# Kernel optimization log

Measured on AMD Instinct MI355X. Metric: run time of the kernel, lower is better.

The kernel has to match this reference:

```python
import jax, jax.numpy as jnp
import numpy as np

SCALE = 16.0 / 8.0  # alpha / rank


def setup_inputs() -> dict:
    key = jax.random.key(0)
    ks = jax.random.split(key, 5)
    d_in, d_out, rank = 4096, 4096, 8
    x = jax.random.normal(ks[0], (4, 2048, d_in), dtype=jnp.float32)
    base_weight = jax.random.normal(ks[1], (d_out, d_in), dtype=jnp.float32) * 0.02
    lora_A = jax.random.normal(ks[2], (rank, d_in), dtype=jnp.float32) * 0.02
    lora_B = jax.random.normal(ks[3], (d_out, rank), dtype=jnp.float32) * 0.02
    bias = jax.random.normal(ks[4], (d_out,), dtype=jnp.float32) * 0.02
    return {"x": x, "base_weight": base_weight, "lora_A": lora_A,
            "lora_B": lora_B, "bias": bias}


def reference(x, base_weight, lora_A, lora_B, bias):
    # weight = base + scale * (B @ A)   -> [d_out, d_in]
    weight = base_weight + SCALE * (lora_B @ lora_A)
    # F.linear: x @ weight.T + bias
    return jnp.einsum('bsi,oi->bso', x, weight) + bias
```

## Files before the change

kernel.cpp:

```cpp
#include <hip/hip_runtime.h>
#include <hip/hip_bf16.h>
#include <cstdio>


using bf16   = __bf16;
using bf16x8 = __attribute__((ext_vector_type(8))) __bf16;
using f32x4  = __attribute__((ext_vector_type(4))) float;

#define BM 256
#define BN 256
#define BK 64
#define WXBLK 2048

__global__ __launch_bounds__(256) void prep_fused(
    const float* __restrict__ x, const float* __restrict__ base,
    const float* __restrict__ A, const float* __restrict__ Bm,
    bf16* __restrict__ Xb, bf16* __restrict__ Wb,
    long n8x, int K, int rank, float scale) {
    if (blockIdx.x < WXBLK) {
        const long stride = (long)WXBLK * 256;
        for (long i = (long)blockIdx.x * 256 + threadIdx.x; i < n8x; i += stride) {
            const float4 a = reinterpret_cast<const float4*>(x)[2 * i];
            const float4 b = reinterpret_cast<const float4*>(x)[2 * i + 1];
            bf16x8 o;
            o[0] = (bf16)a.x; o[1] = (bf16)a.y; o[2] = (bf16)a.z; o[3] = (bf16)a.w;
            o[4] = (bf16)b.x; o[5] = (bf16)b.y; o[6] = (bf16)b.z; o[7] = (bf16)b.w;
            reinterpret_cast<bf16x8*>(Xb)[i] = o;
        }
    } else {
        const int o = blockIdx.x - WXBLK;
        float br[8];
        const int rr = rank < 8 ? rank : 8;
        for (int r = 0; r < rr; ++r) br[r] = scale * Bm[(size_t)o * rank + r];

        const float* brow = base + (size_t)o * K;
        bf16*        wrow = Wb + (size_t)o * K;

        for (int c = threadIdx.x * 8; c < K; c += 256 * 8) {
            float4 s0 = *reinterpret_cast<const float4*>(brow + c);
            float4 s1 = *reinterpret_cast<const float4*>(brow + c + 4);
            if (rank == 8) {
#pragma unroll
                for (int r = 0; r < 8; ++r) {
                    const float4 a0 = *reinterpret_cast<const float4*>(A + (size_t)r * K + c);
                    const float4 a1 = *reinterpret_cast<const float4*>(A + (size_t)r * K + c + 4);
                    s0.x += br[r] * a0.x; s0.y += br[r] * a0.y;
                    s0.z += br[r] * a0.z; s0.w += br[r] * a0.w;
                    s1.x += br[r] * a1.x; s1.y += br[r] * a1.y;
                    s1.z += br[r] * a1.z; s1.w += br[r] * a1.w;
                }
            } else {
                for (int r = 0; r < rank; ++r) {
                    const float b = scale * Bm[(size_t)o * rank + r];
                    const float4 a0 = *reinterpret_cast<const float4*>(A + (size_t)r * K + c);
                    const float4 a1 = *reinterpret_cast<const float4*>(A + (size_t)r * K + c + 4);
                    s0.x += b * a0.x; s0.y += b * a0.y; s0.z += b * a0.z; s0.w += b * a0.w;
                    s1.x += b * a1.x; s1.y += b * a1.y; s1.z += b * a1.z; s1.w += b * a1.w;
                }
            }
            bf16x8 ov;
            ov[0] = (bf16)s0.x; ov[1] = (bf16)s0.y; ov[2] = (bf16)s0.z; ov[3] = (bf16)s0.w;
            ov[4] = (bf16)s1.x; ov[5] = (bf16)s1.y; ov[6] = (bf16)s1.z; ov[7] = (bf16)s1.w;
            *reinterpret_cast<bf16x8*>(wrow + c) = ov;
        }
    }
}

__global__ __launch_bounds__(512, 2) void gemm_2reg(
    const bf16* __restrict__ Xb,
    const bf16* __restrict__ Wb,
    const float* __restrict__ bias,
    float* __restrict__ out,
    int M, int N, int K)
{
    __shared__ __align__(16) bf16 As[2 * 2 * 256 * 32];
    __shared__ __align__(16) bf16 Bs[2 * 2 * 256 * 32];

    const int tid  = threadIdx.x;
    const int lane = tid & 63;
    const int wv   = tid >> 6;
    const int wm   = wv >> 2;
    const int wn   = wv & 3;

    const int nbx = gridDim.x;
    const int nwg = gridDim.x * gridDim.y;
    const int orig = blockIdx.y * nbx + blockIdx.x;
    const int swz = ((nwg & 7) == 0) ? ((orig & 7) * (nwg >> 3) + (orig >> 3)) : orig;
    const int m0 = (swz / nbx) * BM;
    const int n0 = (swz % nbx) * BN;

    const int r16 = lane & 15;
    const int q   = lane >> 4;
    const int cq  = (q ^ ((r16 >> 1) & 3)) * 8;

    const bf16* srcA[2];
    const bf16* srcB[2];
#pragma unroll
    for (int i = 0; i < 2; ++i) {
        const int slot = i * 512 + tid;
        const int row  = slot >> 2;
        const int c    = (tid & 3) ^ ((row >> 1) & 3);
        srcA[i] = Xb + (size_t)(m0 + row) * K + c * 8;
        srcB[i] = Wb + (size_t)(n0 + row) * K + c * 8;
    }
    const int dst0 = (0 * 512 + wv * 64) * 8;
    const int dst1 = (1 * 512 + wv * 64) * 8;

#define STAGE_A(buf, kh, koff)                                                        \
    do {                                                                              \
        __builtin_amdgcn_global_load_lds(                                             \
            (const __attribute__((address_space(1))) void*)(srcA[0] + (koff) + (kh) * 32), \
            (__attribute__((address_space(3))) void*)(As + (buf) * 16384 + (kh) * 8192 + dst0), \
            16, 0, 0);                                                                \
        __builtin_amdgcn_global_load_lds(                                             \
            (const __attribute__((address_space(1))) void*)(srcA[1] + (koff) + (kh) * 32), \
            (__attribute__((address_space(3))) void*)(As + (buf) * 16384 + (kh) * 8192 + dst1), \
            16, 0, 0);                                                                \
    } while (0)
#define STAGE_B(buf, kh, koff)                                                        \
    do {                                                                              \
        __builtin_amdgcn_global_load_lds(                                             \
            (const __attribute__((address_space(1))) void*)(srcB[0] + (koff) + (kh) * 32), \
            (__attribute__((address_space(3))) void*)(Bs + (buf) * 16384 + (kh) * 8192 + dst0), \
            16, 0, 0);                                                                \
        __builtin_amdgcn_global_load_lds(                                             \
            (const __attribute__((address_space(1))) void*)(srcB[1] + (koff) + (kh) * 32), \
            (__attribute__((address_space(3))) void*)(Bs + (buf) * 16384 + (kh) * 8192 + dst1), \
            16, 0, 0);                                                                \
    } while (0)

    int aoff[2][4], boff[4];
#pragma unroll
    for (int mh = 0; mh < 2; ++mh)
#pragma unroll
        for (int f = 0; f < 4; ++f)
            aoff[mh][f] = (wm * 128 + mh * 64 + f * 16 + r16) * 32 + cq;
#pragma unroll
    for (int f = 0; f < 4; ++f)
        boff[f] = (wn * 64 + f * 16 + r16) * 32 + cq;

    f32x4 acc[8][4] = {};

    const int NT = K / BK;

    STAGE_A(0, 0, 0);
    STAGE_B(0, 0, 0);
    STAGE_A(0, 1, 0);
    STAGE_B(0, 1, 0);
    if (NT > 1) {
        STAGE_A(1, 0, BK);
        STAGE_B(1, 0, BK);
        asm volatile("s_waitcnt vmcnt(8)" ::: "memory");
    } else {
        asm volatile("s_waitcnt vmcnt(4)" ::: "memory");
    }
    __builtin_amdgcn_s_barrier();

    for (int t = 0; t < NT; ++t) {
        const int cur   = t & 1;
        const int nxt   = cur ^ 1;
        const int koff1 = (t + 1) * BK;
        const int koff2 = (t + 2) * BK;
        const bool pre1 = (t + 1 < NT);
        const bool pre2 = (t + 2 < NT);
        bf16x8 bf[4], af0[4], af1[4];

        {
            const bf16* Ab = As + cur * 16384;
            const bf16* Bb = Bs + cur * 16384;
#pragma unroll
            for (int f = 0; f < 4; ++f) bf[f]  = *reinterpret_cast<const bf16x8*>(Bb + boff[f]);
#pragma unroll
            for (int f = 0; f < 4; ++f) af0[f] = *reinterpret_cast<const bf16x8*>(Ab + aoff[0][f]);
#pragma unroll
            for (int f = 0; f < 4; ++f) af1[f] = *reinterpret_cast<const bf16x8*>(Ab + aoff[1][f]);
            if (pre1) { STAGE_A(nxt, 1, koff1); STAGE_B(nxt, 1, koff1); }
            asm volatile("s_waitcnt lgkmcnt(4)" ::: "memory");
            __builtin_amdgcn_sched_barrier(0);
            __builtin_amdgcn_s_setprio(1);
#pragma unroll
            for (int f = 0; f < 4; ++f)
#pragma unroll
                for (int n = 0; n < 4; ++n)
                    acc[f][n] = __builtin_amdgcn_mfma_f32_16x16x32_bf16(af0[f], bf[n], acc[f][n], 0, 0, 0);
            __builtin_amdgcn_s_setprio(0);
            asm volatile("s_waitcnt lgkmcnt(0)" ::: "memory");
            __builtin_amdgcn_sched_barrier(0);
            __builtin_amdgcn_s_setprio(1);
#pragma unroll
            for (int f = 0; f < 4; ++f)
#pragma unroll
                for (int n = 0; n < 4; ++n)
                    acc[4 + f][n] = __builtin_amdgcn_mfma_f32_16x16x32_bf16(af1[f], bf[n], acc[4 + f][n], 0, 0, 0);
            __builtin_amdgcn_s_setprio(0);
            if (t == NT - 1) asm volatile("s_waitcnt vmcnt(0)" ::: "memory");
            else             asm volatile("s_waitcnt vmcnt(8)" ::: "memory");
            __builtin_amdgcn_s_barrier();
        }
        {
            const bf16* Ab = As + cur * 16384 + 8192;
            const bf16* Bb = Bs + cur * 16384 + 8192;
#pragma unroll
            for (int f = 0; f < 4; ++f) bf[f]  = *reinterpret_cast<const bf16x8*>(Bb + boff[f]);
#pragma unroll
            for (int f = 0; f < 4; ++f) af0[f] = *reinterpret_cast<const bf16x8*>(Ab + aoff[0][f]);
#pragma unroll
            for (int f = 0; f < 4; ++f) af1[f] = *reinterpret_cast<const bf16x8*>(Ab + aoff[1][f]);
            if (pre2) { STAGE_A(cur, 0, koff2); STAGE_B(cur, 0, koff2); }
            asm volatile("s_waitcnt lgkmcnt(4)" ::: "memory");
            __builtin_amdgcn_sched_barrier(0);
            __builtin_amdgcn_s_setprio(1);
#pragma unroll
            for (int f = 0; f < 4; ++f)
#pragma unroll
                for (int n = 0; n < 4; ++n)
                    acc[f][n] = __builtin_amdgcn_mfma_f32_16x16x32_bf16(af0[f], bf[n], acc[f][n], 0, 0, 0);
            __builtin_amdgcn_s_setprio(0);
            asm volatile("s_waitcnt lgkmcnt(0)" ::: "memory");
            __builtin_amdgcn_sched_barrier(0);
            __builtin_amdgcn_s_setprio(1);
#pragma unroll
            for (int f = 0; f < 4; ++f)
#pragma unroll
                for (int n = 0; n < 4; ++n)
                    acc[4 + f][n] = __builtin_amdgcn_mfma_f32_16x16x32_bf16(af1[f], bf[n], acc[4 + f][n], 0, 0, 0);
            __builtin_amdgcn_s_setprio(0);
            if (t == NT - 2)     asm volatile("s_waitcnt vmcnt(4)" ::: "memory");
            else if (t < NT - 2) asm volatile("s_waitcnt vmcnt(8)" ::: "memory");
            if (t < NT - 1) __builtin_amdgcn_s_barrier();
        }
    }

#pragma unroll
    for (int mf = 0; mf < 8; ++mf) {
        const int gr = m0 + wm * 128 + (mf >> 2) * 64 + (mf & 3) * 16 + q * 4;
#pragma unroll
        for (int nf = 0; nf < 4; ++nf) {
            const int gc = n0 + wn * 64 + nf * 16 + r16;
            const float bv = bias[gc];
#pragma unroll
            for (int r = 0; r < 4; ++r)
                out[(size_t)(gr + r) * N + gc] = acc[mf][nf][r] + bv;
        }
    }
#undef STAGE_A
#undef STAGE_B
}

extern "C" void kernel_launch(void* const* d_in, const int* in_sizes, int n_in,
                              void* d_out, int out_size, void* d_ws, size_t ws_size,
                              hipStream_t stream) {
    const float* x    = (const float*)d_in[0];
    const float* base = (const float*)d_in[1];
    const float* lA   = (const float*)d_in[2];
    const float* lB   = (const float*)d_in[3];
    const float* bias = (const float*)d_in[4];
    float* out = (float*)d_out;

    const int  N    = in_sizes[4];
    const int  rank = in_sizes[3] / N;
    const int  K    = in_sizes[2] / rank;
    const long M    = (long)in_sizes[0] / K;
    const float scale = 16.0f / (float)rank;

    bf16* Xb = (bf16*)d_ws;
    bf16* Wb = Xb + (size_t)M * K;
    const size_t need = ((size_t)M * K + (size_t)N * K) * sizeof(bf16);
    if (ws_size < need) {
        fprintf(stderr, "kernel_launch: ws_size %zu < needed %zu\n", ws_size, need);
        return;
    }

    const long n8x = (long)M * K / 8;
    prep_fused<<<dim3((unsigned)(WXBLK + N)), dim3(256), 0, stream>>>(
        x, base, lA, lB, Xb, Wb, n8x, K, rank, scale);

    gemm_2reg<<<dim3(N / BN, (unsigned)(M / BM)), dim3(512), 0, stream>>>(
        Xb, Wb, bias, out, (int)M, N, K);
}
```

Before: 553.3 us.

## Double-buffer LDS fragment registers to overlap next half-tile reads with MFMA

Restructures the GEMM main loop so each half-K step reads the next half-tile's A/B fragments from LDS into a second register set while the current set feeds the MFMAs. The lgkmcnt/vmcnt waits and barrier placement change to match the new order. The aim is to hide LDS read latency behind matrix math instead of stalling between the two MFMA groups. It doubles fragment register usage (24 bf16x8 registers), which risks register pressure at the 512x2 launch bounds. It also depends on correct manual waitcnt accounting.

```diff
diff --git a/kernel.cpp b/kernel.cpp
--- a/kernel.cpp
+++ b/kernel.cpp
@@ -66,7 +66,7 @@
     }
 }
 
-__global__ __launch_bounds__(512, 2) void gemm_2reg(
+__global__ __launch_bounds__(512, 2) void gemm_rp(
     const bf16* __restrict__ Xb,
     const bf16* __restrict__ Wb,
     const float* __restrict__ bias,
@@ -140,6 +140,8 @@
         boff[f] = (wn * 64 + f * 16 + r16) * 32 + cq;
 
     f32x4 acc[8][4] = {};
+    bf16x8 b0[4], a00[4], a01[4];
+    bf16x8 b1[4], a10[4], a11[4];
 
     const int NT = K / BK;
 
@@ -150,11 +152,21 @@
     if (NT > 1) {
         STAGE_A(1, 0, BK);
         STAGE_B(1, 0, BK);
-        asm volatile("s_waitcnt vmcnt(8)" ::: "memory");
+        asm volatile("s_waitcnt vmcnt(4)" ::: "memory");
     } else {
-        asm volatile("s_waitcnt vmcnt(4)" ::: "memory");
+        asm volatile("s_waitcnt vmcnt(0)" ::: "memory");
     }
     __builtin_amdgcn_s_barrier();
+    {
+        const bf16* Ab = As;
+        const bf16* Bb = Bs;
+#pragma unroll
+        for (int f = 0; f < 4; ++f) b0[f]  = *reinterpret_cast<const bf16x8*>(Bb + boff[f]);
+#pragma unroll
+        for (int f = 0; f < 4; ++f) a00[f] = *reinterpret_cast<const bf16x8*>(Ab + aoff[0][f]);
+#pragma unroll
+        for (int f = 0; f < 4; ++f) a01[f] = *reinterpret_cast<const bf16x8*>(Ab + aoff[1][f]);
+    }
 
     for (int t = 0; t < NT; ++t) {
         const int cur   = t & 1;
@@ -163,71 +175,72 @@
         const int koff2 = (t + 2) * BK;
         const bool pre1 = (t + 1 < NT);
         const bool pre2 = (t + 2 < NT);
-        bf16x8 bf[4], af0[4], af1[4];
-
-        {
-            const bf16* Ab = As + cur * 16384;
-            const bf16* Bb = Bs + cur * 16384;
-#pragma unroll
-            for (int f = 0; f < 4; ++f) bf[f]  = *reinterpret_cast<const bf16x8*>(Bb + boff[f]);
-#pragma unroll
-            for (int f = 0; f < 4; ++f) af0[f] = *reinterpret_cast<const bf16x8*>(Ab + aoff[0][f]);
-#pragma unroll
-            for (int f = 0; f < 4; ++f) af1[f] = *reinterpret_cast<const bf16x8*>(Ab + aoff[1][f]);
-            if (pre1) { STAGE_A(nxt, 1, koff1); STAGE_B(nxt, 1, koff1); }
-            asm volatile("s_waitcnt lgkmcnt(4)" ::: "memory");
-            __builtin_amdgcn_sched_barrier(0);
-            __builtin_amdgcn_s_setprio(1);
-#pragma unroll
-            for (int f = 0; f < 4; ++f)
-#pragma unroll
-                for (int n = 0; n < 4; ++n)
-                    acc[f][n] = __builtin_amdgcn_mfma_f32_16x16x32_bf16(af0[f], bf[n], acc[f][n], 0, 0, 0);
-            __builtin_amdgcn_s_setprio(0);
-            asm volatile("s_waitcnt lgkmcnt(0)" ::: "memory");
-            __builtin_amdgcn_sched_barrier(0);
-            __builtin_amdgcn_s_setprio(1);
-#pragma unroll
-            for (int f = 0; f < 4; ++f)
-#pragma unroll
-                for (int n = 0; n < 4; ++n)
-                    acc[4 + f][n] = __builtin_amdgcn_mfma_f32_16x16x32_bf16(af1[f], bf[n], acc[4 + f][n], 0, 0, 0);
-            __builtin_amdgcn_s_setprio(0);
-            if (t == NT - 1) asm volatile("s_waitcnt vmcnt(0)" ::: "memory");
-            else             asm volatile("s_waitcnt vmcnt(8)" ::: "memory");
-            __builtin_amdgcn_s_barrier();
-        }
+
         {
             const bf16* Ab = As + cur * 16384 + 8192;
             const bf16* Bb = Bs + cur * 16384 + 8192;
 #pragma unroll
-            for (int f = 0; f < 4; ++f) bf[f]  = *reinterpret_cast<const bf16x8*>(Bb + boff[f]);
-#pragma unroll
-            for (int f = 0; f < 4; ++f) af0[f] = *reinterpret_cast<const bf16x8*>(Ab + aoff[0][f]);
-#pragma unroll
-            for (int f = 0; f < 4; ++f) af1[f] = *reinterpret_cast<const bf16x8*>(Ab + aoff[1][f]);
+            for (int f = 0; f < 4; ++f) b1[f]  = *reinterpret_cast<const bf16x8*>(Bb + boff[f]);
+#pragma unroll
+            for (int f = 0; f < 4; ++f) a10[f] = *reinterpret_cast<const bf16x8*>(Ab + aoff[0][f]);
+#pragma unroll
+            for (int f = 0; f < 4; ++f) a11[f] = *reinterpret_cast<const bf16x8*>(Ab + aoff[1][f]);
+            if (pre1) { STAGE_A(nxt, 1, koff1); STAGE_B(nxt, 1, koff1); }
+            __builtin_amdgcn_sched_barrier(0);
+            asm volatile("s_waitcnt lgkmcnt(12)" ::: "memory");
+            __builtin_amdgcn_sched_barrier(0);
+            __builtin_amdgcn_s_setprio(1);
+#pragma unroll
+            for (int f = 0; f < 4; ++f)
+#pragma unroll
+                for (int n = 0; n < 4; ++n)
+                    acc[f][n] = __builtin_amdgcn_mfma_f32_16x16x32_bf16(a00[f], b0[n], acc[f][n], 0, 0, 0);
+#pragma unroll
+            for (int f = 0; f < 4; ++f)
+#pragma unroll
+                for (int n = 0; n < 4; ++n)
+                    acc[4 + f][n] = __builtin_amdgcn_mfma_f32_16x16x32_bf16(a01[f], b0[n], acc[4 + f][n], 0, 0, 0);
+            __builtin_amdgcn_s_setprio(0);
+            __builtin_amdgcn_sched_barrier(0);
+            if (t < NT - 1) {
+                asm volatile("s_waitcnt vmcnt(4)" ::: "memory");
+                __builtin_amdgcn_s_barrier();
+            }
+        }
+        {
+            const bf16* Ab = As + nxt * 16384;
+            const bf16* Bb = Bs + nxt * 16384;
+            if (pre1) {
+#pragma unroll
+                for (int f = 0; f < 4; ++f) b0[f]  = *reinterpret_cast<const bf16x8*>(Bb + boff[f]);
+#pragma unroll
+                for (int f = 0; f < 4; ++f) a00[f] = *reinterpret_cast<const bf16x8*>(Ab + aoff[0][f]);
+#pragma unroll
+                for (int f = 0; f < 4; ++f) a01[f] = *reinterpret_cast<const bf16x8*>(Ab + aoff[1][f]);
+            }
             if (pre2) { STAGE_A(cur, 0, koff2); STAGE_B(cur, 0, koff2); }
-            asm volatile("s_waitcnt lgkmcnt(4)" ::: "memory");
+            __builtin_amdgcn_sched_barrier(0);
+            if (pre1) asm volatile("s_waitcnt lgkmcnt(12)" ::: "memory");
+            else      asm volatile("s_waitcnt lgkmcnt(0)"  ::: "memory");
             __builtin_amdgcn_sched_barrier(0);
             __builtin_amdgcn_s_setprio(1);
 #pragma unroll
             for (int f = 0; f < 4; ++f)
 #pragma unroll
                 for (int n = 0; n < 4; ++n)
-                    acc[f][n] = __builtin_amdgcn_mfma_f32_16x16x32_bf16(af0[f], bf[n], acc[f][n], 0, 0, 0);
+                    acc[f][n] = __builtin_amdgcn_mfma_f32_16x16x32_bf16(a10[f], b1[n], acc[f][n], 0, 0, 0);
+#pragma unroll
+            for (int f = 0; f < 4; ++f)
+#pragma unroll
+                for (int n = 0; n < 4; ++n)
+                    acc[4 + f][n] = __builtin_amdgcn_mfma_f32_16x16x32_bf16(a11[f], b1[n], acc[4 + f][n], 0, 0, 0);
             __builtin_amdgcn_s_setprio(0);
-            asm volatile("s_waitcnt lgkmcnt(0)" ::: "memory");
-            __builtin_amdgcn_sched_barrier(0);
-            __builtin_amdgcn_s_setprio(1);
-#pragma unroll
-            for (int f = 0; f < 4; ++f)
-#pragma unroll
-                for (int n = 0; n < 4; ++n)
-                    acc[4 + f][n] = __builtin_amdgcn_mfma_f32_16x16x32_bf16(af1[f], bf[n], acc[4 + f][n], 0, 0, 0);
-            __builtin_amdgcn_s_setprio(0);
-            if (t == NT - 2)     asm volatile("s_waitcnt vmcnt(4)" ::: "memory");
-            else if (t < NT - 2) asm volatile("s_waitcnt vmcnt(8)" ::: "memory");
-            if (t < NT - 1) __builtin_amdgcn_s_barrier();
+            __builtin_amdgcn_sched_barrier(0);
+            if (t < NT - 1) {
+                if (t == NT - 2) asm volatile("s_waitcnt vmcnt(0)" ::: "memory");
+                else             asm volatile("s_waitcnt vmcnt(4)" ::: "memory");
+                __builtin_amdgcn_s_barrier();
+            }
         }
     }
 
@@ -275,6 +288,6 @@
     prep_fused<<<dim3((unsigned)(WXBLK + N)), dim3(256), 0, stream>>>(
         x, base, lA, lB, Xb, Wb, n8x, K, rank, scale);
 
-    gemm_2reg<<<dim3(N / BN, (unsigned)(M / BM)), dim3(512), 0, stream>>>(
+    gemm_rp<<<dim3(N / BN, (unsigned)(M / BM)), dim3(512), 0, stream>>>(
         Xb, Wb, bias, out, (int)M, N, K);
 }
```

Result: faster. 517.7 us (-6.4%).
